# Performance work log

Measured on AMD Instinct MI355X. Metric: run time of the kernel, lower is better.

The kernel has to match this reference:

```python
import jax, jax.numpy as jnp
import numpy as np

N = 100000          # num_nodes
E = 1250000         # num_edges
H = 64              # node_hidden_size
T = 2               # num_rounds


def setup_inputs() -> dict:
    key = jax.random.key(0)
    ks = jax.random.split(key, 10)
    s = 0.1  # init scale for weights
    return {
        "x": jax.random.normal(ks[0], (N, H), dtype=jnp.float32),
        "edge_index": jax.random.randint(ks[1], (2, E), 0, N, dtype=jnp.int64),
        "edge_attr": jax.random.normal(ks[2], (E, 1), dtype=jnp.float32),
        # message layers: Linear(2H+1 -> H), one per round
        "msg_W": jax.random.normal(ks[3], (T, H, 2 * H + 1), dtype=jnp.float32) * s,
        "msg_b": jax.random.normal(ks[4], (T, H), dtype=jnp.float32) * s,
        # GRUCell params, gate order (r, z, n) as in torch
        "gru_Wih": jax.random.normal(ks[5], (T, 3 * H, H), dtype=jnp.float32) * s,
        "gru_bih": jax.random.normal(ks[6], (T, 3 * H), dtype=jnp.float32) * s,
        "gru_Whh": jax.random.normal(ks[7], (T, 3 * H, H), dtype=jnp.float32) * s,
        "gru_bhh": jax.random.normal(ks[8], (T, 3 * H), dtype=jnp.float32) * s,
    }


def _gru_cell(inp, h, Wih, bih, Whh, bhh):
    # torch.nn.GRUCell math, gate order r, z, n
    gi = inp @ Wih.T + bih   # [N, 3H]
    gh = h @ Whh.T + bhh     # [N, 3H]
    i_r, i_z, i_n = jnp.split(gi, 3, axis=1)
    h_r, h_z, h_n = jnp.split(gh, 3, axis=1)
    r = jax.nn.sigmoid(i_r + h_r)
    z = jax.nn.sigmoid(i_z + h_z)
    n = jnp.tanh(i_n + r * h_n)
    return (1.0 - z) * n + z * h


def reference(x, edge_index, edge_attr, msg_W, msg_b, gru_Wih, gru_bih, gru_Whh, gru_bhh):
    row, col = edge_index[0], edge_index[1]
    num_rounds = msg_W.shape[0]
    for t in range(num_rounds):
        src = x[row]    # [E, H]
        dest = x[col]   # [E, H]
        m_input = jnp.concatenate([dest, src, edge_attr], axis=1)  # [E, 2H+1]
        messages = m_input @ msg_W[t].T + msg_b[t]                 # [E, H]
        agg = jax.ops.segment_sum(messages, row, num_segments=x.shape[0])  # [N, H]
        x = _gru_cell(agg, x, gru_Wih[t], gru_bih[t], gru_Whh[t], gru_bhh[t])
    return x
```

## Files before the change

kernel.cpp:

```cpp
#include <hip/hip_runtime.h>
#include <hip/hip_bf16.h>
#include <hip/hip_fp16.h>

#define H 64
#define CAP 48

typedef __attribute__((ext_vector_type(8))) short short8;
typedef __attribute__((ext_vector_type(4))) float float4v;

__device__ __forceinline__ short f2bf_bits(float f) {
    union { __hip_bfloat16 b; short s; } u;
    u.b = __float2bfloat16(f);
    return u.s;
}
__device__ __forceinline__ float bf2f(unsigned short s) {
    union { unsigned int u; float f; } v;
    v.u = ((unsigned int)s) << 16;
    return v.f;
}
__device__ __forceinline__ void split8(const float* p, short8& hi, short8& lo) {
    float4v f0 = *(const float4v*)p;
    float4v f1 = *(const float4v*)(p + 4);
#pragma unroll
    for (int j = 0; j < 8; j++) {
        float f = (j < 4) ? f0[j] : f1[j - 4];
        short h = f2bf_bits(f);
        float fh = bf2f((unsigned short)h);
        hi[j] = h;
        lo[j] = f2bf_bits(f - fh);
    }
}
__device__ __forceinline__ void zero8(short8& hi, short8& lo) {
#pragma unroll
    for (int j = 0; j < 8; j++) { hi[j] = 0; lo[j] = 0; }
}

#define MFMA(a, b, c) __builtin_amdgcn_mfma_f32_16x16x32_bf16(a, b, c, 0, 0, 0)

__global__ __launch_bounds__(256) void count_prep(
    const int* __restrict__ row, int* __restrict__ deg, int* __restrict__ lpos,
    int E, int EB,
    const float* __restrict__ msg_W,
    const float* __restrict__ Wih, const float* __restrict__ Whh,
    short* __restrict__ msgfrag, short* __restrict__ grufrag, int T)
{
    if ((int)blockIdx.x < EB) {
        int e = blockIdx.x * 256 + threadIdx.x;
        if (e < E) lpos[e] = atomicAdd(&deg[row[e]], 1);
        return;
    }
    const int lane = threadIdx.x & 63;
    int unit = (blockIdx.x - EB) * 4 + (threadIdx.x >> 6);
    const int kq = (lane >> 4) * 8;
    if (unit < T * 16) {
        const int slot = unit & 15, t = unit >> 4;
        const int tile = slot >> 1, ks = slot & 1;
        const float* W = msg_W + (size_t)t * H * 129;
        const int wrow = (tile & 3) * 16 + (lane & 15);
        const int coff = (tile < 4) ? 0 : 64;
        short8 hi, lo;
        split8(W + (size_t)wrow * 129 + coff + ks * 32 + kq, hi, lo);
        short8* out = (short8*)(msgfrag + (size_t)t * 16384);
        out[slot * 64 + lane] = hi;
        out[16 * 64 + slot * 64 + lane] = lo;
    } else {
        unit -= T * 16;
        if (unit >= T * 48) return;
        const int slot = unit % 48, t = unit / 48;
        const int tile = slot >> 1, ks = slot & 1;
        const float* Wp = (tile < 12)
            ? (Wih + (size_t)t * 192 * H + ((size_t)(tile * 16 + (lane & 15))) * H)
            : (Whh + (size_t)t * 192 * H + ((size_t)((tile - 12) * 16 + (lane & 15))) * H);
        short8 hi, lo;
        split8(Wp + ks * 32 + kq, hi, lo);
        short8* out = (short8*)(grufrag + (size_t)t * 49152);
        out[slot * 64 + lane] = hi;
        out[48 * 64 + slot * 64 + lane] = lo;
    }
}

__global__ __launch_bounds__(256) void scatter_cast(
    const int* __restrict__ row, const int* __restrict__ col,
    const float* __restrict__ attr, const int* __restrict__ lpos,
    int2* __restrict__ edata, int E, int EB,
    const float* __restrict__ x_in, __half* __restrict__ xh, int NH8)
{
    if ((int)blockIdx.x < EB) {
        int e = blockIdx.x * 256 + threadIdx.x;
        if (e < E) {
            int p = lpos[e];
            if (p < CAP) {
                int2 v;
                v.x = col[e];
                v.y = __float_as_int(attr[e]);
                edata[(size_t)row[e] * CAP + p] = v;
            }
        }
    } else {
        int i = (blockIdx.x - EB) * 256 + threadIdx.x;
        if (i < NH8) {
            const float* p = x_in + (size_t)i * 8;
            float4v f0 = *(const float4v*)p;
            float4v f1 = *(const float4v*)(p + 4);
            short8 hv;
#pragma unroll
            for (int u = 0; u < 8; u++) {
                float f = (u < 4) ? f0[u] : f1[u - 4];
                hv[u] = __half_as_short(__float2half(f));
            }
            *(short8*)(xh + (size_t)i * 8) = hv;
        }
    }
}

__global__ __launch_bounds__(256) void aggregate(
    const int* __restrict__ deg, const int2* __restrict__ edata,
    const __half* __restrict__ xh,
    short* __restrict__ s_hi, short* __restrict__ s_lo,
    float2* __restrict__ asum2, int N)
{
    const int tid = threadIdx.x, lane = tid & 63, wv = tid >> 6;
    const int g = lane >> 3, cl = lane & 7;
    const int n = (blockIdx.x * 4 + wv) * 8 + g;
    int cnt = 0;
    if (n < N) { cnt = deg[n]; if (cnt > CAP) cnt = CAP; }
    const int2* ebase = edata + (size_t)n * CAP;
    float acc[8] = {0.f,0.f,0.f,0.f,0.f,0.f,0.f,0.f};
    float aacc = 0.f;
    for (int j = 0; j < cnt; j += 8) {
        int2 e[8];
#pragma unroll
        for (int u = 0; u < 8; u++) {
            int idx = j + u; if (idx > cnt - 1) idx = cnt - 1;
            e[u] = ebase[idx];
        }
        short8 h[8];
#pragma unroll
        for (int u = 0; u < 8; u++) {
            int c = e[u].x;
            c = (c < 0) ? 0 : (c >= N ? N - 1 : c);
            h[u] = *(const short8*)(xh + (size_t)c * H + cl * 8);
        }
#pragma unroll
        for (int u = 0; u < 8; u++) {
            const bool val = (j + u < cnt);
            const float w = val ? 1.f : 0.f;
            aacc += val ? __int_as_float(e[u].y) : 0.f;
#pragma unroll
            for (int k = 0; k < 8; k++)
                acc[k] = fmaf(w, __half2float(__ushort_as_half((unsigned short)h[u][k])), acc[k]);
        }
    }
    if (n < N) {
        short8 hi8, lo8;
#pragma unroll
        for (int u = 0; u < 8; u++) {
            float v = acc[u];
            short hbits = f2bf_bits(v);
            hi8[u] = hbits;
            lo8[u] = f2bf_bits(v - bf2f((unsigned short)hbits));
        }
        *(short8*)(s_hi + (size_t)n * H + cl * 8) = hi8;
        *(short8*)(s_lo + (size_t)n * H + cl * 8) = lo8;
        if (cl == 0) asum2[n] = make_float2(aacc, (float)cnt);
    }
}

#define SLD 68
__global__ __launch_bounds__(256) void fused_msg_gru(
    const short* __restrict__ s_hi, const short* __restrict__ s_lo,
    const float2* __restrict__ asum2,
    const float* xf,
    float* x, __half* __restrict__ xh,
    const short* __restrict__ mfrag, const short* __restrict__ gfrag,
    const float* __restrict__ Wt, const float* __restrict__ mb,
    const float* __restrict__ bih, const float* __restrict__ bhh,
    int N, int write_xh)
{
    __shared__ float scratch[4][16 * SLD];
    const int tid = threadIdx.x, lane = tid & 63, wv = tid >> 6;
    const int base = blockIdx.x * 64 + wv * 16;
    if (base >= N) return;
    const int arow = lane & 15;
    const int kq = (lane >> 4) * 8;
    const int colb = lane & 15;
    const int rq4 = (lane >> 4) * 4;
    const int m_a = base + arow;
    const bool mv = (m_a < N);
    const short8* mhi = (const short8*)mfrag;
    const short8* mlo = mhi + 16 * 64;
    const short8* ghi = (const short8*)gfrag;
    const short8* glo = ghi + 48 * 64;
    float* scr = scratch[wv];

    short8 sfh[2], sfl[2], xfh[2], xfl[2];
#pragma unroll
    for (int ks = 0; ks < 2; ks++) {
        if (mv) {
            sfh[ks] = *(const short8*)(s_hi + (size_t)m_a * H + ks * 32 + kq);
            sfl[ks] = *(const short8*)(s_lo + (size_t)m_a * H + ks * 32 + kq);
            split8(xf + (size_t)m_a * H + ks * 32 + kq, xfh[ks], xfl[ks]);
        } else { zero8(sfh[ks], sfl[ks]); zero8(xfh[ks], xfl[ks]); }
    }
    float2 da[4];
#pragma unroll
    for (int r = 0; r < 4; r++) {
        const int m = base + rq4 + r;
        da[r] = (m < N) ? asum2[m] : make_float2(0.f, 0.f);
    }

    float4v accd[4], accs[4];
#pragma unroll
    for (int ct = 0; ct < 4; ct++) {
        accd[ct] = (float4v){0.f, 0.f, 0.f, 0.f};
        accs[ct] = (float4v){0.f, 0.f, 0.f, 0.f};
    }
#pragma unroll
    for (int ks = 0; ks < 2; ks++) {
#pragma unroll
        for (int ct = 0; ct < 4; ct++) {
            short8 bh = mhi[(ct * 2 + ks) * 64 + lane];
            short8 bl = mlo[(ct * 2 + ks) * 64 + lane];
            accd[ct] = MFMA(sfh[ks], bh, accd[ct]);
            accd[ct] = MFMA(sfl[ks], bh, accd[ct]);
            accd[ct] = MFMA(sfh[ks], bl, accd[ct]);
            short8 ch = mhi[((4 + ct) * 2 + ks) * 64 + lane];
            short8 cl8 = mlo[((4 + ct) * 2 + ks) * 64 + lane];
            accs[ct] = MFMA(xfh[ks], ch, accs[ct]);
            accs[ct] = MFMA(xfl[ks], ch, accs[ct]);
            accs[ct] = MFMA(xfh[ks], cl8, accs[ct]);
        }
    }

#pragma unroll
    for (int ct = 0; ct < 4; ct++) {
        const int j = ct * 16 + colb;
        const float bj = mb[j];
        const float wa = Wt[(size_t)j * 129 + 128];
#pragma unroll
        for (int r = 0; r < 4; r++) {
            float v = accd[ct][r] + da[r].y * (accs[ct][r] + bj) + da[r].x * wa;
            scr[(rq4 + r) * SLD + j] = v;
        }
    }
    asm volatile("s_waitcnt lgkmcnt(0)" ::: "memory");
    short8 agh[2], agl[2];
#pragma unroll
    for (int ks = 0; ks < 2; ks++)
        split8(scr + arow * SLD + ks * 32 + kq, agh[ks], agl[ks]);

#pragma unroll
    for (int ct = 0; ct < 4; ct++) {
        float4v ai[3], ao[3];
#pragma unroll
        for (int g2 = 0; g2 < 3; g2++) {
            ai[g2] = (float4v){0.f, 0.f, 0.f, 0.f};
            ao[g2] = (float4v){0.f, 0.f, 0.f, 0.f};
        }
#pragma unroll
        for (int ks = 0; ks < 2; ks++) {
#pragma unroll
            for (int g2 = 0; g2 < 3; g2++) {
                short8 bh = ghi[((g2 * 4 + ct) * 2 + ks) * 64 + lane];
                short8 bl = glo[((g2 * 4 + ct) * 2 + ks) * 64 + lane];
                ai[g2] = MFMA(agh[ks], bh, ai[g2]);
                ai[g2] = MFMA(agl[ks], bh, ai[g2]);
                ai[g2] = MFMA(agh[ks], bl, ai[g2]);
                short8 hh = ghi[((12 + g2 * 4 + ct) * 2 + ks) * 64 + lane];
                short8 hl = glo[((12 + g2 * 4 + ct) * 2 + ks) * 64 + lane];
                ao[g2] = MFMA(xfh[ks], hh, ao[g2]);
                ao[g2] = MFMA(xfl[ks], hh, ao[g2]);
                ao[g2] = MFMA(xfh[ks], hl, ao[g2]);
            }
        }
        const int j = ct * 16 + colb;
        const float b_ir = bih[j], b_iz = bih[64 + j], b_in = bih[128 + j];
        const float b_hr = bhh[j], b_hz = bhh[64 + j], b_hn = bhh[128 + j];
#pragma unroll
        for (int r = 0; r < 4; r++) {
            const int m = base + rq4 + r;
            float ir = ai[0][r] + b_ir;
            float iz = ai[1][r] + b_iz;
            float in_ = ai[2][r] + b_in;
            float hr = ao[0][r] + b_hr;
            float hz = ao[1][r] + b_hz;
            float hn = ao[2][r] + b_hn;
            float rr = 1.f / (1.f + __expf(-(ir + hr)));
            float zz = 1.f / (1.f + __expf(-(iz + hz)));
            float e2 = __expf(2.f * (in_ + rr * hn));
            float nn = 1.f - 2.f / (e2 + 1.f);
            float hold = (m < N) ? xf[(size_t)m * H + j] : 0.f;
            scr[(rq4 + r) * SLD + j] = (1.f - zz) * nn + zz * hold;
        }
    }
    asm volatile("s_waitcnt lgkmcnt(0)" ::: "memory");

    if (mv) {
        float4v o[4];
#pragma unroll
        for (int q4 = 0; q4 < 4; q4++)
            o[q4] = *(const float4v*)(scr + arow * SLD + (lane >> 4) * 16 + q4 * 4);
        float4v* xp = (float4v*)(x + (size_t)m_a * H + (lane >> 4) * 16);
        xp[0] = o[0]; xp[1] = o[1]; xp[2] = o[2]; xp[3] = o[3];
        if (write_xh) {
            short8 hv0, hv1;
#pragma unroll
            for (int u = 0; u < 8; u++) {
                hv0[u] = __half_as_short(__float2half(o[u >> 2][u & 3]));
                hv1[u] = __half_as_short(__float2half(o[2 + (u >> 2)][u & 3]));
            }
            *(short8*)(xh + (size_t)m_a * H + (lane >> 4) * 16) = hv0;
            *(short8*)(xh + (size_t)m_a * H + (lane >> 4) * 16 + 8) = hv1;
        }
    }
}

extern "C" void kernel_launch(void* const* d_in, const int* in_sizes, int n_in,
                              void* d_out, int out_size, void* d_ws, size_t ws_size,
                              hipStream_t stream) {
    const float* x_in  = (const float*)d_in[0];
    const int*   ei    = (const int*)d_in[1];
    const float* attr  = (const float*)d_in[2];
    const float* msg_W = (const float*)d_in[3];
    const float* msg_b = (const float*)d_in[4];
    const float* Wih   = (const float*)d_in[5];
    const float* bih   = (const float*)d_in[6];
    const float* Whh   = (const float*)d_in[7];
    const float* bhh   = (const float*)d_in[8];

    const int N = in_sizes[0] / H;
    const int E = in_sizes[2];
    const int T = in_sizes[4] / H;
    const int* row = ei;
    const int* col = ei + E;

    float*  x       = (float*)d_out;
    short*  s_hi    = (short*)d_ws;
    short*  s_lo    = s_hi + (size_t)N * H;
    int*    lpos    = (int*)s_lo;
    __half* xh      = (__half*)(s_lo + (size_t)N * H);
    float2* asum2   = (float2*)(xh + (size_t)N * H);
    int*    deg     = (int*)(asum2 + N);
    int2*   edata   = (int2*)(deg + N);
    short*  msgfrag = (short*)(edata + (size_t)N * CAP);
    short*  grufrag = msgfrag + (size_t)T * 16384;

    const int eb  = (E + 255) / 256;
    const int nh8 = (N * H) / 8;
    const int cb  = (nh8 + 255) / 256;
    const int pb  = (T * 16 + T * 48 + 3) / 4;

    hipMemsetAsync(deg, 0, (size_t)N * sizeof(int), stream);

    count_prep<<<eb + pb, 256, 0, stream>>>(
        row, deg, lpos, E, eb, msg_W, Wih, Whh, msgfrag, grufrag, T);
    scatter_cast<<<eb + cb, 256, 0, stream>>>(
        row, col, attr, lpos, edata, E, eb, x_in, xh, nh8);

    const int nbq        = (N + 63) / 64;
    const int agg_blocks = (N + 31) / 32;

    for (int t = 0; t < T; t++) {
        aggregate<<<agg_blocks, 256, 0, stream>>>(
            deg, edata, xh, s_hi, s_lo, asum2, N);
        fused_msg_gru<<<nbq, 256, 0, stream>>>(
            s_hi, s_lo, asum2,
            (t == 0) ? x_in : x, x, xh,
            msgfrag + (size_t)t * 16384, grufrag + (size_t)t * 49152,
            msg_W + (size_t)t * H * (2 * H + 1), msg_b + (size_t)t * H,
            bih + (size_t)t * 3 * H, bhh + (size_t)t * 3 * H,
            N, (t + 1 < T) ? 1 : 0);
    }
}
```

Baseline: 343.6 us.

## Replace capped per-node edge buckets with scanned CSR sorted by column slice

Replaces the fixed-capacity (48) per-node edge buckets with an exact CSR built by counting per (row, column-slice) key, a three-stage prefix scan, and a scatter. Edges within a node are grouped by column slice to improve gather locality, and edges beyond the cap are no longer dropped. The GRU hold values are prefetched before the MFMA loops, and those loops are wrapped in s_setprio. In exchange it adds three scan kernels, a larger count array (N*NS entries) and a serial single-block mid scan.

```diff
diff --git a/kernel.cpp b/kernel.cpp
--- a/kernel.cpp
+++ b/kernel.cpp
@@ -3,7 +3,7 @@
 #include <hip/hip_fp16.h>
 
 #define H 64
-#define CAP 48
+#define SLICE_SHIFT 13
 
 typedef __attribute__((ext_vector_type(8))) short short8;
 typedef __attribute__((ext_vector_type(4))) float float4v;
@@ -38,15 +38,19 @@
 #define MFMA(a, b, c) __builtin_amdgcn_mfma_f32_16x16x32_bf16(a, b, c, 0, 0, 0)
 
 __global__ __launch_bounds__(256) void count_prep(
-    const int* __restrict__ row, int* __restrict__ deg, int* __restrict__ lpos,
-    int E, int EB,
+    const int* __restrict__ row, const int* __restrict__ col,
+    int* __restrict__ deg13, int* __restrict__ lpos,
+    int E, int EB, int NS,
     const float* __restrict__ msg_W,
     const float* __restrict__ Wih, const float* __restrict__ Whh,
     short* __restrict__ msgfrag, short* __restrict__ grufrag, int T)
 {
     if ((int)blockIdx.x < EB) {
         int e = blockIdx.x * 256 + threadIdx.x;
-        if (e < E) lpos[e] = atomicAdd(&deg[row[e]], 1);
+        if (e < E) {
+            int key = row[e] * NS + (col[e] >> SLICE_SHIFT);
+            lpos[e] = atomicAdd(&deg13[key], 1);
+        }
         return;
     }
     const int lane = threadIdx.x & 63;
@@ -79,22 +83,74 @@
     }
 }
 
+__global__ __launch_bounds__(256) void scan_block(
+    const int* __restrict__ deg, int* __restrict__ offsets,
+    int* __restrict__ block_sums, int L)
+{
+    __shared__ int s[256];
+    int tid = threadIdx.x, gid = blockIdx.x * 256 + tid;
+    int v = (gid < L) ? deg[gid] : 0;
+    s[tid] = v; __syncthreads();
+    for (int off = 1; off < 256; off <<= 1) {
+        int t = (tid >= off) ? s[tid - off] : 0;
+        __syncthreads();
+        s[tid] += t;
+        __syncthreads();
+    }
+    if (gid < L) offsets[gid] = s[tid] - v;
+    if (tid == 255) block_sums[blockIdx.x] = s[255];
+}
+
+__global__ __launch_bounds__(1024) void scan_mid(int* __restrict__ bsums, int nb)
+{
+    __shared__ int s[1024];
+    __shared__ int carry_s;
+    const int tid = threadIdx.x;
+    if (tid == 0) carry_s = 0;
+    __syncthreads();
+    for (int base = 0; base < nb; base += 1024) {
+        int v = (base + tid < nb) ? bsums[base + tid] : 0;
+        s[tid] = v; __syncthreads();
+        for (int off = 1; off < 1024; off <<= 1) {
+            int t = (tid >= off) ? s[tid - off] : 0;
+            __syncthreads();
+            s[tid] += t;
+            __syncthreads();
+        }
+        int incl = s[tid];
+        int carry0 = carry_s;
+        if (base + tid < nb) bsums[base + tid] = carry0 + incl - v;
+        __syncthreads();
+        if (tid == 1023) carry_s = carry0 + incl;
+        __syncthreads();
+    }
+}
+
+__global__ __launch_bounds__(256) void scan_add(
+    int* __restrict__ offsets, const int* __restrict__ block_sums, int L, int E)
+{
+    int gid = blockIdx.x * 256 + threadIdx.x;
+    if (gid < L) offsets[gid] += block_sums[blockIdx.x];
+    if (gid == 0) offsets[L] = E;
+}
+
 __global__ __launch_bounds__(256) void scatter_cast(
     const int* __restrict__ row, const int* __restrict__ col,
     const float* __restrict__ attr, const int* __restrict__ lpos,
+    const int* __restrict__ offsets, int NS,
     int2* __restrict__ edata, int E, int EB,
     const float* __restrict__ x_in, __half* __restrict__ xh, int NH8)
 {
     if ((int)blockIdx.x < EB) {
         int e = blockIdx.x * 256 + threadIdx.x;
         if (e < E) {
-            int p = lpos[e];
-            if (p < CAP) {
-                int2 v;
-                v.x = col[e];
-                v.y = __float_as_int(attr[e]);
-                edata[(size_t)row[e] * CAP + p] = v;
-            }
+            int c = col[e];
+            int key = row[e] * NS + (c >> SLICE_SHIFT);
+            int p = offsets[key] + lpos[e];
+            int2 v;
+            v.x = c;
+            v.y = __float_as_int(attr[e]);
+            edata[p] = v;
         }
     } else {
         int i = (blockIdx.x - EB) * 256 + threadIdx.x;
@@ -114,7 +170,7 @@
 }
 
 __global__ __launch_bounds__(256) void aggregate(
-    const int* __restrict__ deg, const int2* __restrict__ edata,
+    const int* __restrict__ offsets, int NS, const int2* __restrict__ edata,
     const __half* __restrict__ xh,
     short* __restrict__ s_hi, short* __restrict__ s_lo,
     float2* __restrict__ asum2, int N)
@@ -122,9 +178,12 @@
     const int tid = threadIdx.x, lane = tid & 63, wv = tid >> 6;
     const int g = lane >> 3, cl = lane & 7;
     const int n = (blockIdx.x * 4 + wv) * 8 + g;
-    int cnt = 0;
-    if (n < N) { cnt = deg[n]; if (cnt > CAP) cnt = CAP; }
-    const int2* ebase = edata + (size_t)n * CAP;
+    int beg = 0, cnt = 0;
+    if (n < N) {
+        beg = offsets[(size_t)n * NS];
+        cnt = offsets[(size_t)(n + 1) * NS] - beg;
+    }
+    const int2* ebase = edata + beg;
     float acc[8] = {0.f,0.f,0.f,0.f,0.f,0.f,0.f,0.f};
     float aacc = 0.f;
     for (int j = 0; j < cnt; j += 8) {
@@ -208,6 +267,14 @@
         const int m = base + rq4 + r;
         da[r] = (m < N) ? asum2[m] : make_float2(0.f, 0.f);
     }
+    float holdv[4][4];
+#pragma unroll
+    for (int ct = 0; ct < 4; ct++)
+#pragma unroll
+        for (int r = 0; r < 4; r++) {
+            int mh = base + rq4 + r; if (mh > N - 1) mh = N - 1;
+            holdv[ct][r] = xf[(size_t)mh * H + ct * 16 + colb];
+        }
 
     float4v accd[4], accs[4];
 #pragma unroll
@@ -215,6 +282,7 @@
         accd[ct] = (float4v){0.f, 0.f, 0.f, 0.f};
         accs[ct] = (float4v){0.f, 0.f, 0.f, 0.f};
     }
+    __builtin_amdgcn_s_setprio(1);
 #pragma unroll
     for (int ks = 0; ks < 2; ks++) {
 #pragma unroll
@@ -231,6 +299,7 @@
             accs[ct] = MFMA(xfh[ks], cl8, accs[ct]);
         }
     }
+    __builtin_amdgcn_s_setprio(0);
 
 #pragma unroll
     for (int ct = 0; ct < 4; ct++) {
@@ -257,6 +326,7 @@
             ai[g2] = (float4v){0.f, 0.f, 0.f, 0.f};
             ao[g2] = (float4v){0.f, 0.f, 0.f, 0.f};
         }
+        __builtin_amdgcn_s_setprio(1);
 #pragma unroll
         for (int ks = 0; ks < 2; ks++) {
 #pragma unroll
@@ -273,12 +343,12 @@
                 ao[g2] = MFMA(xfh[ks], hl, ao[g2]);
             }
         }
+        __builtin_amdgcn_s_setprio(0);
         const int j = ct * 16 + colb;
         const float b_ir = bih[j], b_iz = bih[64 + j], b_in = bih[128 + j];
         const float b_hr = bhh[j], b_hz = bhh[64 + j], b_hn = bhh[128 + j];
 #pragma unroll
         for (int r = 0; r < 4; r++) {
-            const int m = base + rq4 + r;
             float ir = ai[0][r] + b_ir;
             float iz = ai[1][r] + b_iz;
             float in_ = ai[2][r] + b_in;
@@ -289,8 +359,7 @@
             float zz = 1.f / (1.f + __expf(-(iz + hz)));
             float e2 = __expf(2.f * (in_ + rr * hn));
             float nn = 1.f - 2.f / (e2 + 1.f);
-            float hold = (m < N) ? xf[(size_t)m * H + j] : 0.f;
-            scr[(rq4 + r) * SLD + j] = (1.f - zz) * nn + zz * hold;
+            scr[(rq4 + r) * SLD + j] = (1.f - zz) * nn + zz * holdv[ct][r];
         }
     }
     asm volatile("s_waitcnt lgkmcnt(0)" ::: "memory");
@@ -333,36 +402,44 @@
     const int T = in_sizes[4] / H;
     const int* row = ei;
     const int* col = ei + E;
+    const int NS = (N + (1 << SLICE_SHIFT) - 1) >> SLICE_SHIFT;
+    const int L  = N * NS;
 
     float*  x       = (float*)d_out;
     short*  s_hi    = (short*)d_ws;
     short*  s_lo    = s_hi + (size_t)N * H;
-    int*    lpos    = (int*)s_lo;
     __half* xh      = (__half*)(s_lo + (size_t)N * H);
     float2* asum2   = (float2*)(xh + (size_t)N * H);
-    int*    deg     = (int*)(asum2 + N);
-    int2*   edata   = (int2*)(deg + N);
-    short*  msgfrag = (short*)(edata + (size_t)N * CAP);
+    int*    deg13   = (int*)(asum2 + N);
+    int*    offsets = deg13 + L;
+    int*    bsums   = offsets + (L + 1);
+    int*    lpos    = bsums + 8192;
+    int2*   edata   = (int2*)(lpos + E);
+    short*  msgfrag = (short*)(edata + E);
     short*  grufrag = msgfrag + (size_t)T * 16384;
 
     const int eb  = (E + 255) / 256;
     const int nh8 = (N * H) / 8;
     const int cb  = (nh8 + 255) / 256;
     const int pb  = (T * 16 + T * 48 + 3) / 4;
-
-    hipMemsetAsync(deg, 0, (size_t)N * sizeof(int), stream);
+    const int nbL = (L + 255) / 256;
+
+    hipMemsetAsync(deg13, 0, (size_t)L * sizeof(int), stream);
 
     count_prep<<<eb + pb, 256, 0, stream>>>(
-        row, deg, lpos, E, eb, msg_W, Wih, Whh, msgfrag, grufrag, T);
+        row, col, deg13, lpos, E, eb, NS, msg_W, Wih, Whh, msgfrag, grufrag, T);
+    scan_block<<<nbL, 256, 0, stream>>>(deg13, offsets, bsums, L);
+    scan_mid<<<1, 1024, 0, stream>>>(bsums, nbL);
+    scan_add<<<nbL, 256, 0, stream>>>(offsets, bsums, L, E);
     scatter_cast<<<eb + cb, 256, 0, stream>>>(
-        row, col, attr, lpos, edata, E, eb, x_in, xh, nh8);
+        row, col, attr, lpos, offsets, NS, edata, E, eb, x_in, xh, nh8);
 
     const int nbq        = (N + 63) / 64;
     const int agg_blocks = (N + 31) / 32;
 
     for (int t = 0; t < T; t++) {
         aggregate<<<agg_blocks, 256, 0, stream>>>(
-            deg, edata, xh, s_hi, s_lo, asum2, N);
+            offsets, NS, edata, xh, s_hi, s_lo, asum2, N);
         fused_msg_gru<<<nbq, 256, 0, stream>>>(
             s_hi, s_lo, asum2,
             (t == 0) ? x_in : x, x, xh,
```

New measurement: 394.2 us. +14.7%, slower.
